# Optimization experiments

Hardware: AMD Instinct MI355X
Metric: run time of the kernel (lower is better)

Reference implementation:

```python
import jax, jax.numpy as jnp
import numpy as np

DIM = 512
QK_DIM = 128
HIDDEN = 1024


def setup_inputs() -> dict:
    key = jax.random.key(0)
    ks = jax.random.split(key, 8)
    b, n = 4, 4096
    x = jax.random.normal(ks[0], (b, n, DIM), dtype=jnp.float32)
    # nn.Linear(dim, hidden*2)
    w_hidden = jax.random.normal(ks[1], (DIM, 2 * HIDDEN), dtype=jnp.float32) / np.sqrt(DIM)
    b_hidden = jnp.zeros((2 * HIDDEN,), dtype=jnp.float32)
    # nn.Linear(dim, qk_dim, bias=False)
    w_qk = jax.random.normal(ks[2], (DIM, QK_DIM), dtype=jnp.float32) / np.sqrt(DIM)
    # OffsetScale params (gamma init 1, beta init 0; randomize slightly for a nontrivial test)
    q_gamma = 1.0 + 0.02 * jax.random.normal(ks[3], (QK_DIM,), dtype=jnp.float32)
    q_beta = 0.02 * jax.random.normal(ks[4], (QK_DIM,), dtype=jnp.float32)
    k_gamma = 1.0 + 0.02 * jax.random.normal(ks[5], (QK_DIM,), dtype=jnp.float32)
    k_beta = 0.02 * jax.random.normal(ks[6], (QK_DIM,), dtype=jnp.float32)
    # nn.Linear(hidden, dim)
    w_out = jax.random.normal(ks[7], (HIDDEN, DIM), dtype=jnp.float32) / np.sqrt(HIDDEN)
    b_out = jnp.zeros((DIM,), dtype=jnp.float32)
    return {
        "x": x,
        "w_hidden": w_hidden, "b_hidden": b_hidden,
        "w_qk": w_qk,
        "q_gamma": q_gamma, "q_beta": q_beta,
        "k_gamma": k_gamma, "k_beta": k_beta,
        "w_out": w_out, "b_out": b_out,
    }


def reference(x, w_hidden, b_hidden, w_qk, q_gamma, q_beta, k_gamma, k_beta, w_out, b_out):
    scale = QK_DIM ** -0.5
    # to_hidden -> chunk into v, gate (NOTE: source applies no activation here)
    hid = jnp.einsum('bnd,dh->bnh', x, w_hidden) + b_hidden  # [b, n, 2*hidden]
    v, gate = jnp.split(hid, 2, axis=-1)                     # each [b, n, hidden]
    qk = jnp.einsum('bnd,de->bne', x, w_qk)                  # [b, n, qk_dim]
    q = qk * q_gamma + q_beta
    k = qk * k_gamma + k_beta
    sim = jnp.einsum('bid,bjd->bij', q, k) * scale           # [b, n, n]
    attn = jnp.square(jax.nn.relu(sim))                      # ReLU^2, no softmax
    out = jnp.einsum('bij,bjh->bih', attn, v)                # [b, n, hidden]
    out = out * gate
    out = jnp.einsum('bnh,hd->bnd', out, w_out) + b_out      # [b, n, dim]
    return out + x  # add_residual=True
```

## Files before the change

### kernel.cpp

```cpp
#include <hip/hip_runtime.h>
#include <hip/hip_bf16.h>

typedef __attribute__((ext_vector_type(8))) short bf16x8;
typedef __attribute__((ext_vector_type(4))) float f32x4;
typedef unsigned short u16;

__device__ __forceinline__ u16 f2b(float f) {
  __hip_bfloat16 h = __float2bfloat16(f);
  return __builtin_bit_cast(unsigned short, h);
}
__device__ __forceinline__ float b2f(u16 u) {
  __hip_bfloat16 h = __builtin_bit_cast(__hip_bfloat16, u);
  return __bfloat162float(h);
}

__device__ __forceinline__ void stage_tile(char* sbase, const char* gbase, int ld_bytes, int tid) {
#pragma unroll
  for (int i = 0; i < 4; ++i) {
    int o = (i * 256 + tid) * 16;
    int row = o >> 7;
    int cb = o & 127;
    int scb = cb ^ ((row & 7) << 4);
    const char* src = gbase + (long)row * ld_bytes + scb;
    __builtin_amdgcn_global_load_lds((const __attribute__((address_space(1))) void*)src,
                                     (__attribute__((address_space(3))) void*)(sbase + o),
                                     16, 0, 0);
  }
}

#define EPI_HID 0
#define EPI_QK 1
#define EPI_ATTN 2
#define EPI_PV 3
#define EPI_OUT 4

template <int EPI>
__global__ __launch_bounds__(256, 2) void gemm_tn(
    const char* Ab, const char* Bb, long sAbat, long sBbat,
    int lda_b, int ldb_b, int nkt,
    u16* o0, u16* o1,
    const float* a0, const float* a1, const float* a2, const float* a3,
    float* fout, const float* xres) {
  __shared__ __align__(16) char lds[32768];
  char* sA = lds;
  char* sB = lds + 16384;
  const int tid = threadIdx.x;
  const int lane = tid & 63;
  const int wave = tid >> 6;
  const int wm = wave >> 1, wn = wave & 1;
  const int l16 = lane & 15, lq = lane >> 4;
  const int bat = blockIdx.z;
  const int row0 = blockIdx.y * 128;
  const int col0 = blockIdx.x * 128;

  const char* Abase = Ab + (long)bat * sAbat + (long)row0 * lda_b;
  const char* Bbase = Bb + (long)bat * sBbat + (long)col0 * ldb_b;

  f32x4 acc[4][4];
#pragma unroll
  for (int i = 0; i < 4; ++i)
#pragma unroll
    for (int j = 0; j < 4; ++j) acc[i][j] = (f32x4){0.f, 0.f, 0.f, 0.f};

  for (int kt = 0; kt < nkt; ++kt) {
    stage_tile(sA, Abase + (long)kt * 128, lda_b, tid);
    stage_tile(sB, Bbase + (long)kt * 128, ldb_b, tid);
    __syncthreads();
#pragma unroll
    for (int kk = 0; kk < 2; ++kk) {
      bf16x8 af[4], bfr[4];
#pragma unroll
      for (int mf = 0; mf < 4; ++mf) {
        int r = wm * 64 + mf * 16 + l16;
        int kb = kk * 64 + lq * 16;
        af[mf] = *(const bf16x8*)(sA + r * 128 + (kb ^ ((r & 7) << 4)));
      }
#pragma unroll
      for (int nf = 0; nf < 4; ++nf) {
        int r = wn * 64 + nf * 16 + l16;
        int kb = kk * 64 + lq * 16;
        bfr[nf] = *(const bf16x8*)(sB + r * 128 + (kb ^ ((r & 7) << 4)));
      }
#pragma unroll
      for (int mf = 0; mf < 4; ++mf)
#pragma unroll
        for (int nf = 0; nf < 4; ++nf)
          acc[mf][nf] = __builtin_amdgcn_mfma_f32_16x16x32_bf16(af[mf], bfr[nf], acc[mf][nf], 0, 0, 0);
    }
    __syncthreads();
  }

#pragma unroll
  for (int mf = 0; mf < 4; ++mf) {
#pragma unroll
    for (int nf = 0; nf < 4; ++nf) {
      const int row = row0 + wm * 64 + mf * 16 + lq * 4;
      const int col = col0 + wn * 64 + nf * 16 + l16;
      f32x4 v = acc[mf][nf];
      if constexpr (EPI == EPI_HID) {
        float bias = a0[col];
        u16* dst = (col < 1024) ? (o0 + (size_t)col * 16384 + row)
                                : (o1 + (size_t)(col - 1024) * 16384 + row);
        ushort4 pk = make_ushort4(f2b(v.x + bias), f2b(v.y + bias), f2b(v.z + bias), f2b(v.w + bias));
        *(ushort4*)dst = pk;
      } else if constexpr (EPI == EPI_QK) {
        float qg = a0[col], qbt = a1[col], kg = a2[col], kbt = a3[col];
#pragma unroll
        for (int i = 0; i < 4; ++i) {
          float t = v[i];
          o0[(size_t)(row + i) * 128 + col] = f2b(t * qg + qbt);
          o1[(size_t)(row + i) * 128 + col] = f2b(t * kg + kbt);
        }
      } else if constexpr (EPI == EPI_ATTN) {
        const float scale = 0.088388347648318447f;
        u16* dst = o0 + (size_t)bat * 4096 * 4096;
#pragma unroll
        for (int i = 0; i < 4; ++i) {
          float t = v[i] * scale;
          t = t > 0.f ? t * t : 0.f;
          dst[(size_t)(row + i) * 4096 + col] = f2b(t);
        }
      } else if constexpr (EPI == EPI_PV) {
        const u16* gt = o1 + (size_t)col * 16384 + (size_t)bat * 4096 + row;
        ushort4 g = *(const ushort4*)gt;
        u16* dst = o0 + (size_t)bat * 4096 * 1024;
        dst[(size_t)(row + 0) * 1024 + col] = f2b(v.x * b2f(g.x));
        dst[(size_t)(row + 1) * 1024 + col] = f2b(v.y * b2f(g.y));
        dst[(size_t)(row + 2) * 1024 + col] = f2b(v.z * b2f(g.z));
        dst[(size_t)(row + 3) * 1024 + col] = f2b(v.w * b2f(g.w));
      } else {
        float bias = a0[col];
#pragma unroll
        for (int i = 0; i < 4; ++i)
          fout[(size_t)(row + i) * 512 + col] = v[i] + bias + xres[(size_t)(row + i) * 512 + col];
      }
    }
  }
}

__global__ void conv_b(const float* in, u16* out, int n) {
  int i = (blockIdx.x * blockDim.x + threadIdx.x) * 4;
  if (i >= n) return;
  float4 f = *(const float4*)(in + i);
  *(ushort4*)(out + i) = make_ushort4(f2b(f.x), f2b(f.y), f2b(f.z), f2b(f.w));
}

__global__ void transpose_b(const float* in, u16* out, int R, int C) {
  int o = blockIdx.x * blockDim.x + threadIdx.x;
  if (o >= R * C) return;
  int c = o / R, r = o - c * R;
  out[o] = f2b(in[(size_t)r * C + c]);
}

extern "C" void kernel_launch(void* const* d_in, const int* in_sizes, int n_in,
                              void* d_out, int out_size, void* d_ws, size_t ws_size,
                              hipStream_t stream) {
  const float* x = (const float*)d_in[0];
  const float* w_hidden = (const float*)d_in[1];
  const float* b_hidden = (const float*)d_in[2];
  const float* w_qk = (const float*)d_in[3];
  const float* q_gamma = (const float*)d_in[4];
  const float* q_beta = (const float*)d_in[5];
  const float* k_gamma = (const float*)d_in[6];
  const float* k_beta = (const float*)d_in[7];
  const float* w_out = (const float*)d_in[8];
  const float* b_out = (const float*)d_in[9];
  float* out = (float*)d_out;

  char* ws = (char*)d_ws;
  size_t off = 0;
  auto alloc = [&](size_t bytes) { char* p = ws + off; off += (bytes + 255) & ~255ull; return p; };
  u16* xb     = (u16*)alloc(16384ull * 512 * 2);
  u16* wh_t   = (u16*)alloc(2048ull * 512 * 2);
  u16* wqk_t  = (u16*)alloc(128ull * 512 * 2);
  u16* wout_t = (u16*)alloc(512ull * 1024 * 2);
  u16* v_t    = (u16*)alloc(1024ull * 16384 * 2);
  u16* g_t    = (u16*)alloc(1024ull * 16384 * 2);
  u16* qb_a   = (u16*)alloc(16384ull * 128 * 2);
  u16* kb_a   = (u16*)alloc(16384ull * 128 * 2);
  u16* attnb  = (u16*)alloc(4ull * 4096 * 4096 * 2);
  u16* out1b  = (u16*)alloc(16384ull * 1024 * 2);

  conv_b<<<(16384 * 512 / 4 + 255) / 256, 256, 0, stream>>>(x, xb, 16384 * 512);
  transpose_b<<<(512 * 2048 + 255) / 256, 256, 0, stream>>>(w_hidden, wh_t, 512, 2048);
  transpose_b<<<(512 * 128 + 255) / 256, 256, 0, stream>>>(w_qk, wqk_t, 512, 128);
  transpose_b<<<(1024 * 512 + 255) / 256, 256, 0, stream>>>(w_out, wout_t, 1024, 512);

  gemm_tn<EPI_HID><<<dim3(16, 128, 1), 256, 0, stream>>>(
      (const char*)xb, (const char*)wh_t, 0, 0, 1024, 1024, 8,
      v_t, g_t, b_hidden, nullptr, nullptr, nullptr, nullptr, nullptr);
  gemm_tn<EPI_QK><<<dim3(1, 128, 1), 256, 0, stream>>>(
      (const char*)xb, (const char*)wqk_t, 0, 0, 1024, 1024, 8,
      qb_a, kb_a, q_gamma, q_beta, k_gamma, k_beta, nullptr, nullptr);
  gemm_tn<EPI_ATTN><<<dim3(32, 32, 4), 256, 0, stream>>>(
      (const char*)qb_a, (const char*)kb_a, 4096ll * 256, 4096ll * 256, 256, 256, 2,
      attnb, nullptr, nullptr, nullptr, nullptr, nullptr, nullptr, nullptr);
  gemm_tn<EPI_PV><<<dim3(8, 32, 4), 256, 0, stream>>>(
      (const char*)attnb, (const char*)v_t, 4096ll * 8192, 8192, 8192, 32768, 64,
      out1b, g_t, nullptr, nullptr, nullptr, nullptr, nullptr, nullptr);
  gemm_tn<EPI_OUT><<<dim3(4, 128, 1), 256, 0, stream>>>(
      (const char*)out1b, (const char*)wout_t, 0, 0, 2048, 2048, 16,
      nullptr, nullptr, b_out, nullptr, nullptr, nullptr, out, x);
}
```

Measured before the change: 356.2 us.

## Add 256x256 double-buffered pipelined GEMM for hidden, attention and PV stages

Introduces a new 512-thread GEMM kernel with 256x256 output tiles, 128KB dynamic LDS double buffering, staged half-tile prefetches interleaved with MFMA phases, s_setprio and explicit vmcnt waits. It also remaps blocks through an XCD-style swizzle for better L2 locality. The hidden projection, QK^T attention and PV GEMMs move to this kernel to raise data reuse per tile and overlap global loads with compute. In exchange it uses far more registers and LDS, lowering occupancy, and the hand-placed waitcnt and barrier scheme is fragile.

Result: faster. 320.6 us (-10.0%).

```diff
diff --git a/kernel.cpp b/kernel.cpp
--- a/kernel.cpp
+++ b/kernel.cpp
@@ -13,6 +13,17 @@
   __hip_bfloat16 h = __builtin_bit_cast(__hip_bfloat16, u);
   return __bfloat162float(h);
 }
+
+#define BAR() __builtin_amdgcn_s_barrier()
+#define LGKM0() do { asm volatile("s_waitcnt lgkmcnt(0)" ::: "memory"); __builtin_amdgcn_sched_barrier(0); } while (0)
+#define VMCNT4() asm volatile("s_waitcnt vmcnt(4)" ::: "memory")
+#define VMCNT0() asm volatile("s_waitcnt vmcnt(0)" ::: "memory")
+
+#define EPI_HID 0
+#define EPI_QK 1
+#define EPI_ATTN 2
+#define EPI_PV 3
+#define EPI_OUT 4
 
 __device__ __forceinline__ void stage_tile(char* sbase, const char* gbase, int ld_bytes, int tid) {
 #pragma unroll
@@ -27,12 +38,6 @@
                                      16, 0, 0);
   }
 }
-
-#define EPI_HID 0
-#define EPI_QK 1
-#define EPI_ATTN 2
-#define EPI_PV 3
-#define EPI_OUT 4
 
 template <int EPI>
 __global__ __launch_bounds__(256, 2) void gemm_tn(
@@ -97,13 +102,7 @@
       const int row = row0 + wm * 64 + mf * 16 + lq * 4;
       const int col = col0 + wn * 64 + nf * 16 + l16;
       f32x4 v = acc[mf][nf];
-      if constexpr (EPI == EPI_HID) {
-        float bias = a0[col];
-        u16* dst = (col < 1024) ? (o0 + (size_t)col * 16384 + row)
-                                : (o1 + (size_t)(col - 1024) * 16384 + row);
-        ushort4 pk = make_ushort4(f2b(v.x + bias), f2b(v.y + bias), f2b(v.z + bias), f2b(v.w + bias));
-        *(ushort4*)dst = pk;
-      } else if constexpr (EPI == EPI_QK) {
+      if constexpr (EPI == EPI_QK) {
         float qg = a0[col], qbt = a1[col], kg = a2[col], kbt = a3[col];
 #pragma unroll
         for (int i = 0; i < 4; ++i) {
@@ -111,6 +110,184 @@
           o0[(size_t)(row + i) * 128 + col] = f2b(t * qg + qbt);
           o1[(size_t)(row + i) * 128 + col] = f2b(t * kg + kbt);
         }
+      } else if constexpr (EPI == EPI_OUT) {
+        float bias = a0[col];
+#pragma unroll
+        for (int i = 0; i < 4; ++i)
+          fout[(size_t)(row + i) * 512 + col] = v[i] + bias + xres[(size_t)(row + i) * 512 + col];
+      }
+    }
+  }
+}
+
+__device__ __forceinline__ void stage_half(char* sbase, const char* gbase, long ld, int tid) {
+#pragma unroll
+  for (int i = 0; i < 2; ++i) {
+    int o = (i * 512 + tid) * 16;
+    int row = o >> 7;
+    int cb = o & 127;
+    int scb = cb ^ ((row & 7) << 4);
+    const char* src = gbase + (long)row * ld + scb;
+    __builtin_amdgcn_global_load_lds((const __attribute__((address_space(1))) void*)src,
+                                     (__attribute__((address_space(3))) void*)(sbase + o),
+                                     16, 0, 0);
+  }
+}
+
+template <int EPI>
+__global__ __launch_bounds__(512, 2) void gemm256(
+    const char* Ab, const char* Bb, long sAbat, long sBbat,
+    long lda, long ldb, int nkt, int nx,
+    u16* o0, u16* o1,
+    const float* a0, float* fout, const float* xres) {
+  extern __shared__ __align__(16) char lds[];
+  const int tid = threadIdx.x;
+  const int lane = tid & 63;
+  const int wave = tid >> 6;
+  const int wm = wave >> 2;
+  const int wn = wave & 3;
+  const int l16 = lane & 15, lq = lane >> 4;
+  const int bat = blockIdx.y;
+
+  const int nwg = gridDim.x;
+  const int qq = nwg >> 3;
+  const int fid = blockIdx.x;
+  const int swz = (fid & 7) * qq + (fid >> 3);
+  const int row0 = (swz / nx) * 256;
+  const int col0 = (swz % nx) * 256;
+
+  const char* gA = Ab + (long)bat * sAbat + (long)row0 * lda;
+  const char* gB = Bb + (long)bat * sBbat + (long)col0 * ldb;
+
+  f32x4 acc[8][4];
+#pragma unroll
+  for (int i = 0; i < 8; ++i)
+#pragma unroll
+    for (int j = 0; j < 4; ++j) acc[i][j] = (f32x4){0.f, 0.f, 0.f, 0.f};
+
+  const int kmask = (l16 & 7) << 4;
+
+  stage_half(lds + 32768, gB, ldb, tid);
+  stage_half(lds + 32768 + 16384, gB + 128 * ldb, ldb, tid);
+  stage_half(lds, gA, lda, tid);
+  stage_half(lds + 16384, gA + 128 * lda, lda, tid);
+  if (nkt > 1) {
+    stage_half(lds + 65536 + 32768, gB + 128, ldb, tid);
+    stage_half(lds + 65536 + 32768 + 16384, gB + 128 * ldb + 128, ldb, tid);
+    VMCNT4();
+  } else {
+    VMCNT0();
+  }
+  BAR();
+
+  bf16x8 af[4][2], bfr[4][2];
+
+  for (int t = 0; t < nkt; ++t) {
+    const char* buf = lds + (t & 1) * 65536;
+    const char* myA = buf + wm * 16384;
+    const char* myB = buf + 32768 + (wn >> 1) * 16384;
+    const int rB = (wn & 1) * 64;
+    char* stA = lds + ((t + 1) & 1) * 65536;
+    char* stB = lds + (t & 1) * 65536 + 32768;
+    const bool sA_ok = (t + 1) < nkt;
+    const bool sB_ok = (t + 2) < nkt;
+
+#pragma unroll
+    for (int nf = 0; nf < 2; ++nf) {
+      int r = rB + nf * 16 + l16;
+#pragma unroll
+      for (int kh = 0; kh < 2; ++kh)
+        bfr[nf][kh] = *(const bf16x8*)(myB + r * 128 + ((kh * 64 + lq * 16) ^ kmask));
+    }
+#pragma unroll
+    for (int mf = 0; mf < 4; ++mf) {
+      int r = mf * 16 + l16;
+#pragma unroll
+      for (int kh = 0; kh < 2; ++kh)
+        af[mf][kh] = *(const bf16x8*)(myA + r * 128 + ((kh * 64 + lq * 16) ^ kmask));
+    }
+    if (sA_ok) stage_half(stA, gA + (long)(t + 1) * 128, lda, tid);
+    BAR();
+    LGKM0();
+    __builtin_amdgcn_s_setprio(1);
+#pragma unroll
+    for (int mf = 0; mf < 4; ++mf)
+#pragma unroll
+      for (int nf = 0; nf < 2; ++nf)
+#pragma unroll
+        for (int kh = 0; kh < 2; ++kh)
+          acc[mf][nf] = __builtin_amdgcn_mfma_f32_16x16x32_bf16(af[mf][kh], bfr[nf][kh], acc[mf][nf], 0, 0, 0);
+    __builtin_amdgcn_s_setprio(0);
+    BAR();
+
+#pragma unroll
+    for (int nf = 2; nf < 4; ++nf) {
+      int r = rB + nf * 16 + l16;
+#pragma unroll
+      for (int kh = 0; kh < 2; ++kh)
+        bfr[nf][kh] = *(const bf16x8*)(myB + r * 128 + ((kh * 64 + lq * 16) ^ kmask));
+    }
+    if (sA_ok) stage_half(stA + 16384, gA + 128 * lda + (long)(t + 1) * 128, lda, tid);
+    BAR();
+    LGKM0();
+    __builtin_amdgcn_s_setprio(1);
+#pragma unroll
+    for (int mf = 0; mf < 4; ++mf)
+#pragma unroll
+      for (int nf = 2; nf < 4; ++nf)
+#pragma unroll
+        for (int kh = 0; kh < 2; ++kh)
+          acc[mf][nf] = __builtin_amdgcn_mfma_f32_16x16x32_bf16(af[mf][kh], bfr[nf][kh], acc[mf][nf], 0, 0, 0);
+    __builtin_amdgcn_s_setprio(0);
+    BAR();
+
+#pragma unroll
+    for (int mf = 0; mf < 4; ++mf) {
+      int r = 64 + mf * 16 + l16;
+#pragma unroll
+      for (int kh = 0; kh < 2; ++kh)
+        af[mf][kh] = *(const bf16x8*)(myA + r * 128 + ((kh * 64 + lq * 16) ^ kmask));
+    }
+    if (sB_ok) stage_half(stB, gB + (long)(t + 2) * 128, ldb, tid);
+    BAR();
+    LGKM0();
+    __builtin_amdgcn_s_setprio(1);
+#pragma unroll
+    for (int mf = 0; mf < 4; ++mf)
+#pragma unroll
+      for (int nf = 2; nf < 4; ++nf)
+#pragma unroll
+        for (int kh = 0; kh < 2; ++kh)
+          acc[4 + mf][nf] = __builtin_amdgcn_mfma_f32_16x16x32_bf16(af[mf][kh], bfr[nf][kh], acc[4 + mf][nf], 0, 0, 0);
+    __builtin_amdgcn_s_setprio(0);
+    BAR();
+
+    if (sB_ok) stage_half(stB + 16384, gB + 128 * ldb + (long)(t + 2) * 128, ldb, tid);
+    __builtin_amdgcn_s_setprio(1);
+#pragma unroll
+    for (int mf = 0; mf < 4; ++mf)
+#pragma unroll
+      for (int nf = 0; nf < 2; ++nf)
+#pragma unroll
+        for (int kh = 0; kh < 2; ++kh)
+          acc[4 + mf][nf] = __builtin_amdgcn_mfma_f32_16x16x32_bf16(af[mf][kh], bfr[nf][kh], acc[4 + mf][nf], 0, 0, 0);
+    __builtin_amdgcn_s_setprio(0);
+    if (sB_ok) { VMCNT4(); } else if (sA_ok) { VMCNT0(); }
+    BAR();
+  }
+
+#pragma unroll
+  for (int mi = 0; mi < 8; ++mi) {
+#pragma unroll
+    for (int ni = 0; ni < 4; ++ni) {
+      const int row = row0 + wm * 128 + mi * 16 + lq * 4;
+      const int col = col0 + wn * 64 + ni * 16 + l16;
+      f32x4 v = acc[mi][ni];
+      if constexpr (EPI == EPI_HID) {
+        float bias = a0[col];
+        u16* dst = (col < 1024) ? (o0 + (size_t)col * 16384 + row)
+                                : (o1 + (size_t)(col - 1024) * 16384 + row);
+        *(ushort4*)dst = make_ushort4(f2b(v.x + bias), f2b(v.y + bias), f2b(v.z + bias), f2b(v.w + bias));
       } else if constexpr (EPI == EPI_ATTN) {
         const float scale = 0.088388347648318447f;
         u16* dst = o0 + (size_t)bat * 4096 * 4096;
@@ -128,11 +305,6 @@
         dst[(size_t)(row + 1) * 1024 + col] = f2b(v.y * b2f(g.y));
         dst[(size_t)(row + 2) * 1024 + col] = f2b(v.z * b2f(g.z));
         dst[(size_t)(row + 3) * 1024 + col] = f2b(v.w * b2f(g.w));
-      } else {
-        float bias = a0[col];
-#pragma unroll
-        for (int i = 0; i < 4; ++i)
-          fout[(size_t)(row + i) * 512 + col] = v[i] + bias + xres[(size_t)(row + i) * 512 + col];
       }
     }
   }
@@ -181,23 +353,27 @@
   u16* attnb  = (u16*)alloc(4ull * 4096 * 4096 * 2);
   u16* out1b  = (u16*)alloc(16384ull * 1024 * 2);
 
+  (void)hipFuncSetAttribute((const void*)gemm256<EPI_HID>, hipFuncAttributeMaxDynamicSharedMemorySize, 131072);
+  (void)hipFuncSetAttribute((const void*)gemm256<EPI_ATTN>, hipFuncAttributeMaxDynamicSharedMemorySize, 131072);
+  (void)hipFuncSetAttribute((const void*)gemm256<EPI_PV>, hipFuncAttributeMaxDynamicSharedMemorySize, 131072);
+
   conv_b<<<(16384 * 512 / 4 + 255) / 256, 256, 0, stream>>>(x, xb, 16384 * 512);
   transpose_b<<<(512 * 2048 + 255) / 256, 256, 0, stream>>>(w_hidden, wh_t, 512, 2048);
   transpose_b<<<(512 * 128 + 255) / 256, 256, 0, stream>>>(w_qk, wqk_t, 512, 128);
   transpose_b<<<(1024 * 512 + 255) / 256, 256, 0, stream>>>(w_out, wout_t, 1024, 512);
 
-  gemm_tn<EPI_HID><<<dim3(16, 128, 1), 256, 0, stream>>>(
-      (const char*)xb, (const char*)wh_t, 0, 0, 1024, 1024, 8,
-      v_t, g_t, b_hidden, nullptr, nullptr, nullptr, nullptr, nullptr);
+  gemm256<EPI_HID><<<dim3(512, 1), 512, 131072, stream>>>(
+      (const char*)xb, (const char*)wh_t, 0, 0, 1024, 1024, 8, 8,
+      v_t, g_t, b_hidden, nullptr, nullptr);
   gemm_tn<EPI_QK><<<dim3(1, 128, 1), 256, 0, stream>>>(
       (const char*)xb, (const char*)wqk_t, 0, 0, 1024, 1024, 8,
       qb_a, kb_a, q_gamma, q_beta, k_gamma, k_beta, nullptr, nullptr);
-  gemm_tn<EPI_ATTN><<<dim3(32, 32, 4), 256, 0, stream>>>(
-      (const char*)qb_a, (const char*)kb_a, 4096ll * 256, 4096ll * 256, 256, 256, 2,
-      attnb, nullptr, nullptr, nullptr, nullptr, nullptr, nullptr, nullptr);
-  gemm_tn<EPI_PV><<<dim3(8, 32, 4), 256, 0, stream>>>(
-      (const char*)attnb, (const char*)v_t, 4096ll * 8192, 8192, 8192, 32768, 64,
-      out1b, g_t, nullptr, nullptr, nullptr, nullptr, nullptr, nullptr);
+  gemm256<EPI_ATTN><<<dim3(256, 4), 512, 131072, stream>>>(
+      (const char*)qb_a, (const char*)kb_a, 4096ll * 256, 4096ll * 256, 256, 256, 2, 16,
+      attnb, nullptr, nullptr, nullptr, nullptr);
+  gemm256<EPI_PV><<<dim3(64, 4), 512, 131072, stream>>>(
+      (const char*)attnb, (const char*)v_t, 4096ll * 8192, 8192, 8192, 32768, 64, 4,
+      out1b, g_t, nullptr, nullptr, nullptr);
   gemm_tn<EPI_OUT><<<dim3(4, 128, 1), 256, 0, stream>>>(
       (const char*)out1b, (const char*)wout_t, 0, 0, 2048, 2048, 16,
       nullptr, nullptr, b_out, nullptr, nullptr, nullptr, out, x);
```
